# Performance work log

Measured on AMD Instinct MI355X. Metric: run time of the kernel, lower is better.

## Reference

```python
import jax, jax.numpy as jnp
import numpy as np

B, D, H, K = 8192, 1280, 16384, 64


def setup_inputs() -> dict:
    key = jax.random.key(0)
    k1, k2, k3 = jax.random.split(key, 3)
    x = jax.random.normal(k1, (B, D), dtype=jnp.float32)
    # encoder weight [hidden_dim, input_dim] (torch Linear layout)
    W_enc = jax.random.normal(k2, (H, D), dtype=jnp.float32) * (1.0 / np.sqrt(D))
    b_enc = jnp.zeros((H,), dtype=jnp.float32)
    # decoder weight [input_dim, hidden_dim], unit-norm columns scaled by 0.1
    W_dec = jax.random.normal(k3, (D, H), dtype=jnp.float32)
    W_dec = 0.1 * W_dec / jnp.linalg.norm(W_dec, axis=0, keepdims=True)
    b_dec = jnp.zeros((D,), dtype=jnp.float32)
    b_pre = jnp.zeros((D,), dtype=jnp.float32)
    return {"x": x, "W_enc": W_enc, "b_enc": b_enc, "W_dec": W_dec,
            "b_dec": b_dec, "b_pre": b_pre, "k": K}


def reference(x, W_enc, b_enc, W_dec, b_dec, b_pre, k):
    # --- encode ---
    x_centered = x - b_pre                                   # [B, D]
    pre = jnp.einsum('bd,hd->bh', x_centered, W_enc) + b_enc  # [B, H]
    vals, idx = jax.lax.top_k(pre, k)                        # [B, k]
    rows = jnp.arange(pre.shape[0])[:, None]                 # [B, 1]
    hidden = jnp.zeros_like(pre).at[rows, idx].set(jax.nn.relu(vals))  # [B, H]
    # --- decode ---
    reconstructed = jnp.einsum('bh,dh->bd', hidden, W_dec) + b_dec + b_pre
    # --- losses ---
    reconstruction_loss = jnp.mean((reconstructed - x) ** 2)
    l0 = jnp.mean(jnp.sum((hidden > 0).astype(jnp.float32), axis=-1))
    sparsity_loss = jnp.array(0.0, dtype=jnp.float32)
    loss = reconstruction_loss
    return reconstructed, hidden, loss, reconstruction_loss, sparsity_loss, l0
```

## Files before the change

### kernel.cpp

```cpp
#include <hip/hip_runtime.h>
#include <hip/hip_bf16.h>

constexpr int K_MAX    = 128;
constexpr int A_MAX    = 256;
constexpr int CAND_MAX = 512;
constexpr int BM = 128, BN = 128, BKF = 16;
constexpr int NBITER = 42;
constexpr int D_MAX   = 2048;
constexpr int H_FIX   = 16384;

typedef __attribute__((ext_vector_type(8))) short bf16x8;
typedef __attribute__((ext_vector_type(8))) unsigned short u16x8;
typedef __attribute__((ext_vector_type(4))) float f32x4;

__device__ inline unsigned short f2bf(float f) {
  unsigned u = __float_as_uint(f);
  return (unsigned short)((u + 0x7fff + ((u >> 16) & 1)) >> 16);
}
__device__ inline unsigned short key_of(float f) {
  unsigned short b = f2bf(f);
  return b ^ ((b & 0x8000) ? 0xFFFF : 0x8000);
}
__device__ inline float val_of_key(unsigned short kk) {
  unsigned short b = (kk & 0x8000) ? (unsigned short)(kk ^ 0x8000)
                                   : (unsigned short)(kk ^ 0xFFFF);
  return __uint_as_float(((unsigned)b) << 16);
}
__device__ inline float bf2f(unsigned short b) {
  return __uint_as_float(((unsigned)b) << 16);
}

__device__ inline int lds_slot(int r, int c) {
  return ((r >> 1) << 4) | ((r & 1) << 3) | (c ^ ((r >> 1) & 7));
}

__global__ __launch_bounds__(256) void prep_xb(
    const float* __restrict__ x, const float* __restrict__ b_pre,
    unsigned short* __restrict__ Xb, int D, size_t total4)
{
  for (size_t i = blockIdx.x * 256 + threadIdx.x; i < total4; i += (size_t)gridDim.x * 256) {
    const size_t e = i * 4;
    const int d = (int)(e % D);
    float4 xv = *reinterpret_cast<const float4*>(x + e);
    float4 bp = *reinterpret_cast<const float4*>(b_pre + d);
    ushort4 o;
    o.x = f2bf(xv.x - bp.x); o.y = f2bf(xv.y - bp.y);
    o.z = f2bf(xv.z - bp.z); o.w = f2bf(xv.w - bp.w);
    *reinterpret_cast<ushort4*>(Xb + e) = o;
  }
}

__global__ __launch_bounds__(256) void prep_wb(
    const float* __restrict__ W, unsigned short* __restrict__ Wb, size_t total4)
{
  for (size_t i = blockIdx.x * 256 + threadIdx.x; i < total4; i += (size_t)gridDim.x * 256) {
    const size_t e = i * 4;
    float4 wv = *reinterpret_cast<const float4*>(W + e);
    ushort4 o;
    o.x = f2bf(wv.x); o.y = f2bf(wv.y); o.z = f2bf(wv.z); o.w = f2bf(wv.w);
    *reinterpret_cast<ushort4*>(Wb + e) = o;
  }
}

__global__ __launch_bounds__(512, 2) void enc_gemm_bf16(
    const unsigned short* __restrict__ Xb, const unsigned short* __restrict__ Wb,
    const float* __restrict__ b_enc, float* __restrict__ pre, int D, int H)
{
  __shared__ unsigned short As[2][2048 * 8];
  __shared__ unsigned short Bs[2][2048 * 8];
  const int tid  = threadIdx.x;
  const int wave = tid >> 6, lane = tid & 63;
  const int m0 = blockIdx.y * 256, n0 = blockIdx.x * 256;
  const int wm = (wave >> 1) * 64;
  const int wn = (wave & 1) * 128;
  const int l16 = lane & 15, lhi = lane >> 4;

  f32x4 acc[4][8];
#pragma unroll
  for (int i = 0; i < 4; ++i)
#pragma unroll
    for (int j = 0; j < 8; ++j) acc[i][j] = (f32x4){0.f, 0.f, 0.f, 0.f};

  const int NT = D / 64;

  auto stageA = [&](int buf, int h, int kb) {
#pragma unroll
    for (int i = 0; i < 2; ++i) {
      const int idx = i * 512 + wave * 64 + lane;
      const int sr = idx >> 4, u = idx & 15;
      const int r  = (sr << 1) | (u >> 3);
      const int ch = (u & 7) ^ (sr & 7);
      __builtin_amdgcn_global_load_lds(
          (const __attribute__((address_space(1))) unsigned int*)
              (Xb + (size_t)(m0 + h * 128 + r) * D + kb + ch * 8),
          (__attribute__((address_space(3))) unsigned int*)
              (&As[buf][(size_t)(h * 1024 + idx) * 8]), 16, 0, 0);
    }
  };
  auto stageBq = [&](int buf, int q, int kb) {
    const int s  = (q & 1) * 512 + wave * 64 + lane;
    const int sr = s >> 4, u = s & 15;
    const int r  = (sr << 1) | (u >> 3);
    const int ch = (u & 7) ^ (sr & 7);
    __builtin_amdgcn_global_load_lds(
        (const __attribute__((address_space(1))) unsigned int*)
            (Wb + (size_t)(n0 + (q >> 1) * 128 + r) * D + kb + ch * 8),
        (__attribute__((address_space(3))) unsigned int*)
            (&Bs[buf][(size_t)((q >> 1) * 1024 + s) * 8]), 16, 0, 0);
  };
  auto readA = [&](int buf, int mi, int kk) -> bf16x8 {
    const int gr = wm + mi * 16 + l16;
    return *reinterpret_cast<const bf16x8*>(
        &As[buf][(size_t)((gr >> 7) * 1024 + lds_slot(gr & 127, kk * 4 + lhi)) * 8]);
  };
  auto readB = [&](int buf, int ni, int kk) -> bf16x8 {
    const int gr = wn + ni * 16 + l16;
    return *reinterpret_cast<const bf16x8*>(
        &Bs[buf][(size_t)((gr >> 7) * 1024 + lds_slot(gr & 127, kk * 4 + lhi)) * 8]);
  };

  stageA(0, 0, 0); stageA(0, 1, 0);
  stageBq(0, 0, 0); stageBq(0, 2, 0);
  stageBq(0, 1, 0); stageBq(0, 3, 0);

  int cur = 0;
  for (int t = 0; t < NT; ++t) {
    const int nxt = cur ^ 1;
    const int kb1 = (t + 1) * 64;
    const bool more = (t + 1 < NT);

    bf16x8 af[4][2], bf[2][2];

    asm volatile("s_waitcnt vmcnt(2)" ::: "memory");
    __builtin_amdgcn_s_barrier();
#pragma unroll
    for (int mi = 0; mi < 4; ++mi)
#pragma unroll
      for (int kk = 0; kk < 2; ++kk) af[mi][kk] = readA(cur, mi, kk);
#pragma unroll
    for (int j = 0; j < 2; ++j)
#pragma unroll
      for (int kk = 0; kk < 2; ++kk) bf[j][kk] = readB(cur, j, kk);
    if (more) stageA(nxt, 0, kb1);
    __builtin_amdgcn_s_setprio(1);
#pragma unroll
    for (int mi = 0; mi < 4; ++mi)
#pragma unroll
      for (int j = 0; j < 2; ++j)
#pragma unroll
        for (int kk = 0; kk < 2; ++kk)
          acc[mi][j] = __builtin_amdgcn_mfma_f32_16x16x32_bf16(af[mi][kk], bf[j][kk], acc[mi][j], 0, 0, 0);
    __builtin_amdgcn_s_setprio(0);

#pragma unroll
    for (int j = 0; j < 2; ++j)
#pragma unroll
      for (int kk = 0; kk < 2; ++kk) bf[j][kk] = readB(cur, 2 + j, kk);
    if (more) stageA(nxt, 1, kb1);
    __builtin_amdgcn_s_setprio(1);
#pragma unroll
    for (int mi = 0; mi < 4; ++mi)
#pragma unroll
      for (int j = 0; j < 2; ++j)
#pragma unroll
        for (int kk = 0; kk < 2; ++kk)
          acc[mi][2 + j] = __builtin_amdgcn_mfma_f32_16x16x32_bf16(af[mi][kk], bf[j][kk], acc[mi][2 + j], 0, 0, 0);
    __builtin_amdgcn_s_setprio(0);

    if (more) { asm volatile("s_waitcnt vmcnt(4)" ::: "memory"); }
    else      { asm volatile("s_waitcnt vmcnt(0)" ::: "memory"); }
    __builtin_amdgcn_s_barrier();
#pragma unroll
    for (int j = 0; j < 2; ++j)
#pragma unroll
      for (int kk = 0; kk < 2; ++kk) bf[j][kk] = readB(cur, 4 + j, kk);
    if (more) { stageBq(nxt, 0, kb1); stageBq(nxt, 2, kb1); }
    __builtin_amdgcn_s_setprio(1);
#pragma unroll
    for (int mi = 0; mi < 4; ++mi)
#pragma unroll
      for (int j = 0; j < 2; ++j)
#pragma unroll
        for (int kk = 0; kk < 2; ++kk)
          acc[mi][4 + j] = __builtin_amdgcn_mfma_f32_16x16x32_bf16(af[mi][kk], bf[j][kk], acc[mi][4 + j], 0, 0, 0);
    __builtin_amdgcn_s_setprio(0);

#pragma unroll
    for (int j = 0; j < 2; ++j)
#pragma unroll
      for (int kk = 0; kk < 2; ++kk) bf[j][kk] = readB(cur, 6 + j, kk);
    if (more) { stageBq(nxt, 1, kb1); stageBq(nxt, 3, kb1); }
    __builtin_amdgcn_s_setprio(1);
#pragma unroll
    for (int mi = 0; mi < 4; ++mi)
#pragma unroll
      for (int j = 0; j < 2; ++j)
#pragma unroll
        for (int kk = 0; kk < 2; ++kk)
          acc[mi][6 + j] = __builtin_amdgcn_mfma_f32_16x16x32_bf16(af[mi][kk], bf[j][kk], acc[mi][6 + j], 0, 0, 0);
    __builtin_amdgcn_s_setprio(0);

    cur = nxt;
  }

#pragma unroll
  for (int ni = 0; ni < 8; ++ni) {
    const int n = n0 + wn + ni * 16 + l16;
    const float be = b_enc[n];
#pragma unroll
    for (int mi = 0; mi < 4; ++mi) {
      const int mbase = m0 + wm + mi * 16 + lhi * 4;
#pragma unroll
      for (int r = 0; r < 4; ++r) {
        unsigned short* prow = (unsigned short*)(pre + (size_t)(mbase + r) * H);
        prow[n] = key_of(acc[mi][ni][r] + be);
      }
    }
  }
}

__global__ __launch_bounds__(256) void select_refine(
    const float* __restrict__ X, const float* __restrict__ b_pre,
    const float* __restrict__ W, const float* __restrict__ b_enc,
    float* __restrict__ hidden, int* __restrict__ tk_idx, float* __restrict__ tk_val,
    const int* __restrict__ kptr, int D, float delta)
{
  constexpr int H = H_FIX, NC = H_FIX / (256 * 8);
  __shared__ int    hist[4096];
  __shared__ int    chunk[256];
  __shared__ int    misc[8];
  __shared__ float  xr[D_MAX];
  __shared__ double asv[A_MAX];
  __shared__ int    aix[A_MAX];

  const int tid = threadIdx.x, b = blockIdx.x;
  const int k = min(*kptr, K_MAX);
  float* hrow = hidden + (size_t)b * H;
  const unsigned short* krow = (const unsigned short*)hrow;

  if (tid < 8) misc[tid] = 0;
  for (int i = tid; i < 4096; i += 256) hist[i] = 0;

  u16x8 kv[NC];
#pragma unroll
  for (int i = 0; i < NC; ++i)
    kv[i] = *reinterpret_cast<const u16x8*>(krow + ((size_t)i * 256 + tid) * 8);
  __syncthreads();

  const float4 z4 = {0.f, 0.f, 0.f, 0.f};
  for (int i = tid; i < (H >> 2); i += 256)
    reinterpret_cast<float4*>(hrow)[i] = z4;
  for (int d = tid; d < D; d += 256) xr[d] = X[(size_t)b * D + d] - b_pre[d];

#pragma unroll
  for (int i = 0; i < NC; ++i)
#pragma unroll
    for (int j = 0; j < 8; ++j)
      atomicAdd(&hist[((unsigned)(unsigned short)kv[i][j]) >> 4], 1);
  __syncthreads();

  int csum = 0;
#pragma unroll
  for (int j = 0; j < 16; ++j) csum += hist[tid * 16 + j];
  chunk[tid] = csum;
  __syncthreads();
  int gt = 0;
  for (int j = tid + 1; j < 256; ++j) gt += chunk[j];
  {
    int run = gt;
#pragma unroll
    for (int j = 15; j >= 0; --j) {
      const int hc = hist[tid * 16 + j];
      if (run < k && k <= run + hc) { misc[0] = tid * 16 + j; misc[1] = run; }
      run += hc;
    }
  }
  __syncthreads();
  const int b1 = misc[0];
  if (tid < 16) chunk[tid] = 0;
  __syncthreads();
#pragma unroll
  for (int i = 0; i < NC; ++i)
#pragma unroll
    for (int j = 0; j < 8; ++j) {
      const unsigned kk = (unsigned)(unsigned short)kv[i][j];
      if ((int)(kk >> 4) == b1) atomicAdd(&chunk[kk & 15], 1);
    }
  __syncthreads();
  if (tid == 0) {
    int run = misc[1];
    int K16 = b1 << 4;
    for (int j = 15; j >= 0; --j) {
      const int c = chunk[j];
      if (run < k && k <= run + c) K16 = (b1 << 4) | j;
      run += c;
    }
    const float v_lo = val_of_key((unsigned short)K16);
    const float v_hi = val_of_key((unsigned short)min(K16 + 1, 65535));
    const float ulp = v_hi - v_lo;
    const float vs = v_hi + delta;
    const float va = v_lo - ulp - delta;
    int ks = key_of(vs); if (val_of_key((unsigned short)ks) > vs) --ks;
    int ka = key_of(va); if (val_of_key((unsigned short)ka) < va) ++ka;
    misc[2] = ks; misc[3] = ka;
  }
  __syncthreads();
  const unsigned ks = (unsigned)misc[2], ka = (unsigned)misc[3];

#pragma unroll
  for (int i = 0; i < NC; ++i)
#pragma unroll
    for (int j = 0; j < 8; ++j) {
      const unsigned kk = (unsigned)(unsigned short)kv[i][j];
      if (kk > ks) {
        const int p = atomicAdd(&misc[4], 1);
        if (p < k) {
          const int h = (i * 256 + tid) * 8 + j;
          const float v = val_of_key((unsigned short)kk);
          const float rv = (v > 0.f) ? v : 0.f;
          hrow[h] = rv;
          tk_idx[(size_t)b * K_MAX + p] = h;
          tk_val[(size_t)b * K_MAX + p] = rv;
        }
      } else if (kk >= ka) {
        const int p = atomicAdd(&misc[5], 1);
        if (p < A_MAX) aix[p] = (i * 256 + tid) * 8 + j;
      }
    }
  __syncthreads();
  const int S = min(misc[4], k);
  const int A = min(misc[5], A_MAX);

  const int wid = tid >> 6, lane = tid & 63;
  for (int c = wid; c < A; c += 4) {
    const int h = aix[c];
    const float* wr = W + (size_t)h * D;
    double s0 = 0.0, s1 = 0.0;
    int i = lane;
    for (; i + 64 < D; i += 128) {
      s0 += (double)xr[i] * (double)wr[i];
      s1 += (double)xr[i + 64] * (double)wr[i + 64];
    }
    if (i < D) s0 += (double)xr[i] * (double)wr[i];
    double s = s0 + s1;
    for (int off = 32; off; off >>= 1) s += __shfl_xor(s, off);
    if (lane == 0) asv[c] = s + (double)b_enc[h];
  }
  __syncthreads();

  const int m = k - S;
  for (int c = tid; c < A; c += 256) {
    const double v = asv[c];
    const int h = aix[c];
    int r = 0;
    for (int j = 0; j < A; ++j) {
      const double vj = asv[j];
      r += ((vj > v) || (vj == v && aix[j] < h)) ? 1 : 0;
    }
    if (r < m) {
      const float rv = (v > 0.0) ? (float)v : 0.f;
      hrow[h] = rv;
      tk_idx[(size_t)b * K_MAX + S + r] = h;
      tk_val[(size_t)b * K_MAX + S + r] = rv;
    }
  }
}

__global__ __launch_bounds__(256) void enc_gemm_f32(
    const float* __restrict__ X, const float* __restrict__ W,
    const float* __restrict__ b_enc, const float* __restrict__ b_pre,
    float* __restrict__ pre, int D, int H)
{
  __shared__ float As[BKF][BM + 4];
  __shared__ float Bs[BKF][BN + 4];
  const int tid = threadIdx.x;
  const int m0 = blockIdx.y * BM;
  const int n0 = blockIdx.x * BN;
  const int tx = tid & 15, ty = tid >> 4;
  float acc[8][8];
#pragma unroll
  for (int i = 0; i < 8; ++i)
#pragma unroll
    for (int j = 0; j < 8; ++j) acc[i][j] = 0.f;

  for (int kb = 0; kb < D; kb += BKF) {
#pragma unroll
    for (int t = 0; t < 2; ++t) {
      const int f4i = tid + t * 256;
      const int row = f4i >> 2;
      const int kq  = (f4i & 3) << 2;
      float4 xv = *reinterpret_cast<const float4*>(X + (size_t)(m0 + row) * D + kb + kq);
      float4 bp = *reinterpret_cast<const float4*>(b_pre + kb + kq);
      As[kq + 0][row] = xv.x - bp.x; As[kq + 1][row] = xv.y - bp.y;
      As[kq + 2][row] = xv.z - bp.z; As[kq + 3][row] = xv.w - bp.w;
      float4 wv = *reinterpret_cast<const float4*>(W + (size_t)(n0 + row) * D + kb + kq);
      Bs[kq + 0][row] = wv.x; Bs[kq + 1][row] = wv.y;
      Bs[kq + 2][row] = wv.z; Bs[kq + 3][row] = wv.w;
    }
    __syncthreads();
#pragma unroll
    for (int kk = 0; kk < BKF; ++kk) {
      float4 a0 = *reinterpret_cast<const float4*>(&As[kk][ty * 8]);
      float4 a1 = *reinterpret_cast<const float4*>(&As[kk][ty * 8 + 4]);
      float4 b0 = *reinterpret_cast<const float4*>(&Bs[kk][tx * 8]);
      float4 b1 = *reinterpret_cast<const float4*>(&Bs[kk][tx * 8 + 4]);
      float av[8] = {a0.x, a0.y, a0.z, a0.w, a1.x, a1.y, a1.z, a1.w};
      float bv[8] = {b0.x, b0.y, b0.z, b0.w, b1.x, b1.y, b1.z, b1.w};
#pragma unroll
      for (int i = 0; i < 8; ++i)
#pragma unroll
        for (int j = 0; j < 8; ++j) acc[i][j] += av[i] * bv[j];
    }
    __syncthreads();
  }
#pragma unroll
  for (int i = 0; i < 8; ++i) {
    const size_t m = (size_t)(m0 + ty * 8 + i);
#pragma unroll
    for (int j = 0; j < 8; j += 4) {
      const int n = n0 + tx * 8 + j;
      float4 o;
      o.x = acc[i][j + 0] + b_enc[n + 0];
      o.y = acc[i][j + 1] + b_enc[n + 1];
      o.z = acc[i][j + 2] + b_enc[n + 2];
      o.w = acc[i][j + 3] + b_enc[n + 3];
      *reinterpret_cast<float4*>(pre + m * H + n) = o;
    }
  }
}

__global__ __launch_bounds__(256) void topk_refine(
    const float* __restrict__ X, const float* __restrict__ b_pre,
    const float* __restrict__ W, const float* __restrict__ b_enc,
    float* __restrict__ hidden, int* __restrict__ tk_idx, float* __restrict__ tk_val,
    const int* __restrict__ kptr, int D, int H, float margin)
{
  extern __shared__ char smem_raw[];
  double* cand_val = reinterpret_cast<double*>(smem_raw);
  float*  xr       = reinterpret_cast<float*>(cand_val + CAND_MAX);
  int*    cand_idx = reinterpret_cast<int*>(xr + D);
  int*    misc     = cand_idx + CAND_MAX;

  const int tid = threadIdx.x;
  const int b = blockIdx.x;
  const int k = min(*kptr, K_MAX);
  float* hrow = hidden + (size_t)b * H;

  for (int i = tid; i < NBITER + 2; i += 256) misc[i] = 0;
  for (int d = tid; d < D; d += 256) xr[d] = X[(size_t)b * D + d] - b_pre[d];

  float f[64];
#pragma unroll
  for (int i = 0; i < 16; ++i) {
    const int base = i * 1024 + tid * 4;
    float4 v = {-3e38f, -3e38f, -3e38f, -3e38f};
    if (base + 3 < H) v = *reinterpret_cast<const float4*>(hrow + base);
    f[4 * i + 0] = v.x; f[4 * i + 1] = v.y; f[4 * i + 2] = v.z; f[4 * i + 3] = v.w;
  }
  __syncthreads();

  float lo = -1e4f, hi = 1e4f;
  for (int it = 0; it < NBITER; ++it) {
    const float mid = 0.5f * (lo + hi);
    int cnt = 0;
#pragma unroll
    for (int j = 0; j < 64; ++j) cnt += (f[j] >= mid) ? 1 : 0;
    for (int off = 32; off; off >>= 1) cnt += __shfl_xor(cnt, off);
    if ((tid & 63) == 0) atomicAdd(&misc[it], cnt);
    __syncthreads();
    if (misc[it] >= k) lo = mid; else hi = mid;
  }

  const float thresh = lo - margin;
#pragma unroll
  for (int j = 0; j < 64; ++j) {
    if (f[j] >= thresh) {
      const int h = (j >> 2) * 1024 + tid * 4 + (j & 3);
      if (h < H) {
        int pos = atomicAdd(&misc[NBITER], 1);
        if (pos < CAND_MAX) cand_idx[pos] = h;
      }
    }
  }
  __syncthreads();
  const int C = min(misc[NBITER], CAND_MAX);

  const int wid = tid >> 6, lane = tid & 63;
  for (int c = wid; c < C; c += 4) {
    const int h = cand_idx[c];
    const float* wr = W + (size_t)h * D;
    double s = 0.0;
    for (int i = lane; i < D; i += 64) s += (double)xr[i] * (double)wr[i];
    for (int off = 32; off; off >>= 1) s += __shfl_xor(s, off);
    if (lane == 0) cand_val[c] = s + (double)b_enc[h];
  }
  __syncthreads();

  const float4 z4 = {0.f, 0.f, 0.f, 0.f};
  for (int i = tid; i < (H >> 2); i += 256)
    reinterpret_cast<float4*>(hrow)[i] = z4;
  __syncthreads();

  for (int c = tid; c < C; c += 256) {
    const double v = cand_val[c];
    const int h = cand_idx[c];
    int r = 0;
    for (int j = 0; j < C; ++j) {
      const double vj = cand_val[j];
      r += ((vj > v) || (vj == v && cand_idx[j] < h)) ? 1 : 0;
    }
    if (r < k) {
      const float rv = (v > 0.0) ? (float)v : 0.f;
      hrow[h] = rv;
      tk_idx[(size_t)b * K_MAX + r] = h;
      tk_val[(size_t)b * K_MAX + r] = rv;
    }
  }
}

__global__ __launch_bounds__(256) void transpose_wdec_bf16(
    const float* __restrict__ Wsrc, unsigned short* __restrict__ WT, int D, int H)
{
  __shared__ float tile[32][33];
  const int c  = threadIdx.x & 31;
  const int r0 = threadIdx.x >> 5;
  const int h0 = blockIdx.x * 32;
  const int d0 = blockIdx.y * 32;
#pragma unroll
  for (int r = r0; r < 32; r += 8) {
    const int d = d0 + r, h = h0 + c;
    if (d < D && h < H) tile[r][c] = Wsrc[(size_t)d * H + h];
  }
  __syncthreads();
#pragma unroll
  for (int r = r0; r < 32; r += 8) {
    const int h = h0 + r, d = d0 + c;
    if (h < H && d < D) WT[(size_t)h * D + d] = f2bf(tile[c][r]);
  }
}

__global__ __launch_bounds__(256) void decode_loss2(
    const float* __restrict__ X, const float* __restrict__ b_pre,
    const float* __restrict__ b_dec, const unsigned short* __restrict__ WTb,
    const int* __restrict__ tk_idx, const float* __restrict__ tk_val,
    const int* __restrict__ kptr,
    float* __restrict__ recon, double* __restrict__ row_ssq, int D)
{
  __shared__ int   sidx[2][K_MAX];
  __shared__ float sval[2][K_MAX];
  __shared__ double sd[4];
  const int tid = threadIdx.x;
  const int half = tid >> 7, lt = tid & 127;
  const int b = blockIdx.x * 2 + half;
  const int k = min(*kptr, K_MAX);
  if (lt < k) {
    sidx[half][lt] = tk_idx[(size_t)b * K_MAX + lt];
    sval[half][lt] = tk_val[(size_t)b * K_MAX + lt];
  }
  __syncthreads();

  double ssq = 0.0;
  const int D8 = D >> 3;
  for (int dc = lt; dc < D8; dc += 128) {
    const int d = dc * 8;
    float a[8];
#pragma unroll
    for (int q = 0; q < 2; ++q) {
      float4 bd = *reinterpret_cast<const float4*>(b_dec + d + q * 4);
      float4 bp = *reinterpret_cast<const float4*>(b_pre + d + q * 4);
      a[q * 4 + 0] = bd.x + bp.x; a[q * 4 + 1] = bd.y + bp.y;
      a[q * 4 + 2] = bd.z + bp.z; a[q * 4 + 3] = bd.w + bp.w;
    }
#pragma unroll 4
    for (int j = 0; j < k; ++j) {
      const u16x8 w = *reinterpret_cast<const u16x8*>(WTb + (size_t)sidx[half][j] * D + d);
      const float s = sval[half][j];
#pragma unroll
      for (int e = 0; e < 8; ++e) a[e] += s * bf2f((unsigned short)w[e]);
    }
#pragma unroll
    for (int q = 0; q < 2; ++q) {
      float4 o = {a[q * 4 + 0], a[q * 4 + 1], a[q * 4 + 2], a[q * 4 + 3]};
      *reinterpret_cast<float4*>(recon + (size_t)b * D + d + q * 4) = o;
    }
#pragma unroll
    for (int e = 0; e < 8; ++e) {
      const double df = (double)a[e] - (double)X[(size_t)b * D + d + e];
      ssq += df * df;
    }
  }
  for (int off = 32; off; off >>= 1) ssq += __shfl_xor(ssq, off);
  if ((tid & 63) == 0) sd[tid >> 6] = ssq;
  __syncthreads();
  if (tid == 0) row_ssq[blockIdx.x * 2 + 0] = sd[0] + sd[1];
  if (tid == 128) row_ssq[blockIdx.x * 2 + 1] = sd[2] + sd[3];
}

__global__ __launch_bounds__(256) void decode_loss(
    const float* __restrict__ X, const float* __restrict__ b_pre,
    const float* __restrict__ b_dec, const float* __restrict__ Wfull,
    const int* __restrict__ tk_idx, const float* __restrict__ tk_val,
    const int* __restrict__ kptr,
    float* __restrict__ recon, double* __restrict__ row_ssq, int D, int H)
{
  __shared__ int   sidx[K_MAX];
  __shared__ float sval[K_MAX];
  __shared__ double sd[4];
  const int tid = threadIdx.x, b = blockIdx.x;
  const int k = min(*kptr, K_MAX);
  if (tid < k) {
    sidx[tid] = tk_idx[(size_t)b * K_MAX + tid];
    sval[tid] = tk_val[(size_t)b * K_MAX + tid];
  }
  __syncthreads();
  double ssq = 0.0;
  for (int d = tid; d < D; d += 256) {
    float a = b_dec[d] + b_pre[d];
#pragma unroll 4
    for (int j = 0; j < k; ++j) a += sval[j] * Wfull[(size_t)d * H + sidx[j]];
    recon[(size_t)b * D + d] = a;
    const double diff = (double)a - (double)X[(size_t)b * D + d];
    ssq += diff * diff;
  }
  for (int off = 32; off; off >>= 1) ssq += __shfl_xor(ssq, off);
  if ((tid & 63) == 0) sd[tid >> 6] = ssq;
  __syncthreads();
  if (tid == 0) row_ssq[b] = sd[0] + sd[1] + sd[2] + sd[3];
}

__global__ __launch_bounds__(256) void finalize_part(
    const double* __restrict__ row_ssq, const float* __restrict__ tk_val,
    const int* __restrict__ kptr, double* __restrict__ part_s, int* __restrict__ part_c,
    int Bdim, int rows_per_blk)
{
  __shared__ double sd[4];
  __shared__ int si[4];
  const int tid = threadIdx.x;
  const int k = min(*kptr, K_MAX);
  const int b0 = blockIdx.x * rows_per_blk;
  const int b1 = min(b0 + rows_per_blk, Bdim);
  double s = 0.0;
  for (int i = b0 + tid; i < b1; i += 256) s += row_ssq[i];
  int cnt = 0;
  const int total = (b1 - b0) * k;
  for (int i = tid; i < total; i += 256) {
    const int bb = b0 + i / k, j = i - (i / k) * k;
    cnt += (tk_val[(size_t)bb * K_MAX + j] > 0.f) ? 1 : 0;
  }
  for (int off = 32; off; off >>= 1) { s += __shfl_xor(s, off); cnt += __shfl_xor(cnt, off); }
  if ((tid & 63) == 0) { sd[tid >> 6] = s; si[tid >> 6] = cnt; }
  __syncthreads();
  if (tid == 0) {
    part_s[blockIdx.x] = sd[0] + sd[1] + sd[2] + sd[3];
    part_c[blockIdx.x] = si[0] + si[1] + si[2] + si[3];
  }
}

__global__ __launch_bounds__(64) void finalize_k2(
    const double* __restrict__ part_s, const int* __restrict__ part_c,
    float* __restrict__ scalars, int nparts, int Bdim, int D)
{
  const int tid = threadIdx.x;
  double s = (tid < nparts) ? part_s[tid] : 0.0;
  int cnt = (tid < nparts) ? part_c[tid] : 0;
  for (int off = 32; off; off >>= 1) { s += __shfl_xor(s, off); cnt += __shfl_xor(cnt, off); }
  if (tid == 0) {
    const double rl = s / ((double)Bdim * (double)D);
    scalars[0] = (float)rl;
    scalars[1] = (float)rl;
    scalars[2] = 0.f;
    scalars[3] = (float)((double)cnt / Bdim);
  }
}

extern "C" void kernel_launch(void* const* d_in, const int* in_sizes, int n_in,
                              void* d_out, int out_size, void* d_ws, size_t ws_size,
                              hipStream_t stream)
{
  const float* x     = (const float*)d_in[0];
  const float* W_enc = (const float*)d_in[1];
  const float* b_enc = (const float*)d_in[2];
  const float* W_dec = (const float*)d_in[3];
  const float* b_dec = (const float*)d_in[4];
  const float* b_pre = (const float*)d_in[5];
  const int*   kptr  = (const int*)d_in[6];

  const int D = in_sizes[4];
  const int H = in_sizes[2];
  const int B = in_sizes[0] / D;

  float* recon   = (float*)d_out;
  float* hidden  = recon + (size_t)B * D;
  float* scalars = hidden + (size_t)B * H;

  size_t off = 0;
  int* tk_idx = (int*)((char*)d_ws + off);        off += (size_t)B * K_MAX * sizeof(int);
  float* tk_val = (float*)((char*)d_ws + off);    off += (size_t)B * K_MAX * sizeof(float);
  off = (off + 7) & ~(size_t)7;
  double* row_ssq = (double*)((char*)d_ws + off); off += (size_t)B * sizeof(double);
  double* part_s = (double*)((char*)d_ws + off);  off += 64 * sizeof(double);
  int* part_c = (int*)((char*)d_ws + off);        off += 64 * sizeof(int);
  off = (off + 7) & ~(size_t)7;

  unsigned short* Xb = (unsigned short*)((char*)d_ws + off);
  off += (size_t)B * D * sizeof(unsigned short);
  unsigned short* Wb = (unsigned short*)((char*)d_ws + off);
  off += (size_t)H * D * sizeof(unsigned short);
  unsigned short* WTb = (unsigned short*)((char*)d_ws + off);
  off += (size_t)D * H * sizeof(unsigned short);
  const int useFAST = (off <= ws_size) ? 1 : 0;

  const bool fast_ok = (D % 64 == 0) && (D % 8 == 0) && (D <= D_MAX) &&
                       (H == H_FIX) && (B % 256 == 0);

  if (useFAST && fast_ok) {
    const size_t tx4 = (size_t)B * D / 4, tw4 = (size_t)H * D / 4;
    prep_xb<<<2048, 256, 0, stream>>>(x, b_pre, Xb, D, tx4);
    prep_wb<<<2048, 256, 0, stream>>>(W_enc, Wb, tw4);
    dim3 gg(H / 256, B / 256);
    enc_gemm_bf16<<<gg, 512, 0, stream>>>(Xb, Wb, b_enc, hidden, D, H);
    select_refine<<<B, 256, 0, stream>>>(x, b_pre, W_enc, b_enc, hidden,
                                         tk_idx, tk_val, kptr, D, 0.05f);
    transpose_wdec_bf16<<<dim3((H + 31) / 32, (D + 31) / 32), 256, 0, stream>>>(W_dec, WTb, D, H);
    decode_loss2<<<B / 2, 256, 0, stream>>>(x, b_pre, b_dec, WTb,
                                            tk_idx, tk_val, kptr, recon, row_ssq, D);
  } else {
    dim3 gg(H / BN, B / BM);
    enc_gemm_f32<<<gg, 256, 0, stream>>>(x, W_enc, b_enc, b_pre, hidden, D, H);
    const size_t sh = CAND_MAX * sizeof(double) + (size_t)D * sizeof(float)
                    + CAND_MAX * sizeof(int) + (NBITER + 8) * sizeof(int);
    topk_refine<<<B, 256, sh, stream>>>(x, b_pre, W_enc, b_enc, hidden,
                                        tk_idx, tk_val, kptr, D, H, 1e-3f);
    decode_loss<<<B, 256, 0, stream>>>(x, b_pre, b_dec, W_dec,
                                       tk_idx, tk_val, kptr, recon, row_ssq, D, H);
  }

  const int rpb = (B + 63) / 64;
  finalize_part<<<64, 256, 0, stream>>>(row_ssq, tk_val, kptr, part_s, part_c, B, rpb);
  finalize_k2<<<1, 64, 0, stream>>>(part_s, part_c, scalars, 64, B, D);
}
```

Measured before the change: 1.052 ms.

## Split top-k selection into key classification and refine/scatter kernels

The fused select_refine kernel is split in two. The first kernel builds the histogram and writes the indices of sure and ambiguous candidates to global workspace. The second kernel loads x and recomputes the ambiguous candidates' dot products in fp64, then scatters the results. This lowers shared-memory and register pressure per kernel, which may raise occupancy, at the cost of an extra launch and a round trip of the candidate lists through global memory.

Result: faster. 998.8 us (-5.0%).

```diff
diff --git a/kernel.cpp b/kernel.cpp
--- a/kernel.cpp
+++ b/kernel.cpp
@@ -2,6 +2,7 @@
 #include <hip/hip_bf16.h>
 
 constexpr int K_MAX    = 128;
+constexpr int S_MAX    = 128;
 constexpr int A_MAX    = 256;
 constexpr int CAND_MAX = 512;
 constexpr int BM = 128, BN = 128, BKF = 16;
@@ -219,19 +220,16 @@
   }
 }
 
-__global__ __launch_bounds__(256) void select_refine(
-    const float* __restrict__ X, const float* __restrict__ b_pre,
-    const float* __restrict__ W, const float* __restrict__ b_enc,
-    float* __restrict__ hidden, int* __restrict__ tk_idx, float* __restrict__ tk_val,
-    const int* __restrict__ kptr, int D, float delta)
+__global__ __launch_bounds__(256) void topk_classify_keys(
+    float* __restrict__ hidden,
+    int* __restrict__ sure_ix, float* __restrict__ sure_val, int* __restrict__ sure_cnt,
+    int* __restrict__ amb_ix, int* __restrict__ amb_cnt,
+    const int* __restrict__ kptr, float delta)
 {
   constexpr int H = H_FIX, NC = H_FIX / (256 * 8);
-  __shared__ int    hist[4096];
-  __shared__ int    chunk[256];
-  __shared__ int    misc[8];
-  __shared__ float  xr[D_MAX];
-  __shared__ double asv[A_MAX];
-  __shared__ int    aix[A_MAX];
+  __shared__ int hist[4096];
+  __shared__ int chunk[256];
+  __shared__ int misc[8];
 
   const int tid = threadIdx.x, b = blockIdx.x;
   const int k = min(*kptr, K_MAX);
@@ -250,7 +248,6 @@
   const float4 z4 = {0.f, 0.f, 0.f, 0.f};
   for (int i = tid; i < (H >> 2); i += 256)
     reinterpret_cast<float4*>(hrow)[i] = z4;
-  for (int d = tid; d < D; d += 256) xr[d] = X[(size_t)b * D + d] - b_pre[d];
 
 #pragma unroll
   for (int i = 0; i < NC; ++i)
@@ -314,22 +311,54 @@
       const unsigned kk = (unsigned)(unsigned short)kv[i][j];
       if (kk > ks) {
         const int p = atomicAdd(&misc[4], 1);
-        if (p < k) {
+        if (p < S_MAX) {
           const int h = (i * 256 + tid) * 8 + j;
-          const float v = val_of_key((unsigned short)kk);
-          const float rv = (v > 0.f) ? v : 0.f;
-          hrow[h] = rv;
-          tk_idx[(size_t)b * K_MAX + p] = h;
-          tk_val[(size_t)b * K_MAX + p] = rv;
+          sure_ix[(size_t)b * S_MAX + p] = h;
+          sure_val[(size_t)b * S_MAX + p] = val_of_key((unsigned short)kk);
         }
       } else if (kk >= ka) {
         const int p = atomicAdd(&misc[5], 1);
-        if (p < A_MAX) aix[p] = (i * 256 + tid) * 8 + j;
+        if (p < A_MAX) amb_ix[(size_t)b * A_MAX + p] = (i * 256 + tid) * 8 + j;
       }
     }
   __syncthreads();
-  const int S = min(misc[4], k);
-  const int A = min(misc[5], A_MAX);
+  if (tid == 0) {
+    sure_cnt[b] = min(misc[4], S_MAX);
+    amb_cnt[b]  = min(misc[5], A_MAX);
+  }
+}
+
+__global__ __launch_bounds__(256) void refine_scatter(
+    const float* __restrict__ X, const float* __restrict__ b_pre,
+    const float* __restrict__ W, const float* __restrict__ b_enc,
+    const int* __restrict__ sure_ix, const float* __restrict__ sure_val,
+    const int* __restrict__ sure_cnt,
+    const int* __restrict__ amb_ix, const int* __restrict__ amb_cnt,
+    const int* __restrict__ kptr,
+    float* __restrict__ hidden, int* __restrict__ tk_idx, float* __restrict__ tk_val, int D)
+{
+  constexpr int H = H_FIX;
+  __shared__ float  xr[D_MAX];
+  __shared__ double asv[A_MAX];
+  __shared__ int    aix[A_MAX];
+  const int tid = threadIdx.x, b = blockIdx.x;
+  const int k = min(*kptr, K_MAX);
+  const int S = min(min(sure_cnt[b], S_MAX), k);
+  const int A = min(amb_cnt[b], A_MAX);
+  float* hrow = hidden + (size_t)b * H;
+
+  for (int d = tid; d < D; d += 256) xr[d] = X[(size_t)b * D + d] - b_pre[d];
+  for (int c = tid; c < A; c += 256) aix[c] = amb_ix[(size_t)b * A_MAX + c];
+
+  for (int i = tid; i < S; i += 256) {
+    const int h = sure_ix[(size_t)b * S_MAX + i];
+    const float v = sure_val[(size_t)b * S_MAX + i];
+    const float rv = (v > 0.f) ? v : 0.f;
+    hrow[h] = rv;
+    tk_idx[(size_t)b * K_MAX + i] = h;
+    tk_val[(size_t)b * K_MAX + i] = rv;
+  }
+  __syncthreads();
 
   const int wid = tid >> 6, lane = tid & 63;
   for (int c = wid; c < A; c += 4) {
@@ -708,9 +737,15 @@
   off += (size_t)H * D * sizeof(unsigned short);
   unsigned short* WTb = (unsigned short*)((char*)d_ws + off);
   off += (size_t)D * H * sizeof(unsigned short);
+
+  int* sure_ix = (int*)((char*)d_ws + off);       off += (size_t)B * S_MAX * sizeof(int);
+  float* sure_val = (float*)((char*)d_ws + off);  off += (size_t)B * S_MAX * sizeof(float);
+  int* sure_cnt = (int*)((char*)d_ws + off);      off += (size_t)B * sizeof(int);
+  int* amb_ix = (int*)((char*)d_ws + off);        off += (size_t)B * A_MAX * sizeof(int);
+  int* amb_cnt = (int*)((char*)d_ws + off);       off += (size_t)B * sizeof(int);
   const int useFAST = (off <= ws_size) ? 1 : 0;
 
-  const bool fast_ok = (D % 64 == 0) && (D % 8 == 0) && (D <= D_MAX) &&
+  const bool fast_ok = (D % 64 == 0) && (D <= D_MAX) &&
                        (H == H_FIX) && (B % 256 == 0);
 
   if (useFAST && fast_ok) {
@@ -719,8 +754,12 @@
     prep_wb<<<2048, 256, 0, stream>>>(W_enc, Wb, tw4);
     dim3 gg(H / 256, B / 256);
     enc_gemm_bf16<<<gg, 512, 0, stream>>>(Xb, Wb, b_enc, hidden, D, H);
-    select_refine<<<B, 256, 0, stream>>>(x, b_pre, W_enc, b_enc, hidden,
-                                         tk_idx, tk_val, kptr, D, 0.05f);
+    topk_classify_keys<<<B, 256, 0, stream>>>(hidden, sure_ix, sure_val, sure_cnt,
+                                              amb_ix, amb_cnt, kptr, 0.05f);
+    refine_scatter<<<B, 256, 0, stream>>>(x, b_pre, W_enc, b_enc,
+                                          sure_ix, sure_val, sure_cnt,
+                                          amb_ix, amb_cnt, kptr,
+                                          hidden, tk_idx, tk_val, D);
     transpose_wdec_bf16<<<dim3((H + 31) / 32, (D + 31) / 32), 256, 0, stream>>>(W_dec, WTb, D, H);
     decode_loss2<<<B / 2, 256, 0, stream>>>(x, b_pre, b_dec, WTb,
                                             tk_idx, tk_val, kptr, recon, row_ssq, D);
```
